# Optimization experiments

Hardware: AMD Instinct MI355X
Metric: run time of the kernel (lower is better)

Reference implementation:

```python
import jax, jax.numpy as jnp
import numpy as np

N = 100000      # nodes
E = 1600000     # edges (avg degree 16)
D_IN = 128
D_OUT = 128


def setup_inputs() -> dict:
    key = jax.random.key(0)
    k_x, k_e, k_w1, k_w2 = jax.random.split(key, 4)
    x = jax.random.normal(k_x, (N, D_IN), dtype=jnp.float32)
    edge_index = jax.random.randint(k_e, (2, E), 0, N, dtype=jnp.int64)
    # xavier_uniform for Linear weights, zero biases (as in reset_parameters)
    lim1 = float(np.sqrt(6.0 / (D_IN + D_OUT)))
    lim2 = float(np.sqrt(6.0 / (D_OUT + D_OUT)))
    W1 = jax.random.uniform(k_w1, (D_IN, D_OUT), jnp.float32, -lim1, lim1)
    b1 = jnp.zeros((D_OUT,), jnp.float32)
    W2 = jax.random.uniform(k_w2, (D_OUT, D_OUT), jnp.float32, -lim2, lim2)
    b2 = jnp.zeros((D_OUT,), jnp.float32)
    eps = jnp.zeros((1,), jnp.float32)  # trainable eps, init 0
    return {"x": x, "edge_index": edge_index, "W1": W1, "b1": b1,
            "W2": W2, "b2": b2, "eps": eps}


def reference(x, edge_index, W1, b1, W2, b2, eps):
    src, dst = edge_index[0], edge_index[1]
    # adj_t.matmul(x): agg[i] = sum_{j in N(i)} x[j]  (gather + scatter-add)
    agg = jax.ops.segment_sum(x[src], dst, num_segments=N)  # [N, D_IN]
    h = (1.0 + eps) * x + agg                                 # eps residual
    h = jax.nn.relu(h @ W1 + b1)                              # Linear + ReLU
    return h @ W2 + b2                                        # Linear
```

## Files before the change

### kernel.cpp

```cpp
#include <hip/hip_runtime.h>

#define DFEAT 128
#define NA 512
#define CELLW 20
#define CAPAB 19
#define MAXBKT 512
#define CAPH 2560
#define OVCAP 32768

typedef __attribute__((ext_vector_type(8))) short short8v;
typedef __attribute__((ext_vector_type(4))) float f32x4;
typedef __attribute__((ext_vector_type(4))) unsigned short ushort4v;

__device__ __forceinline__ unsigned short f2bf(float f) {
    union { float f; unsigned u; } cv; cv.f = f;
    unsigned u = cv.u + 0x7fffu + ((cv.u >> 16) & 1u);
    return (unsigned short)(u >> 16);
}
__device__ __forceinline__ float bf2f(unsigned short h) {
    union { unsigned u; float f; } cv; cv.u = ((unsigned)h) << 16; return cv.f;
}
__device__ __forceinline__ int load_idx(const void* eiv, int is64, size_t i) {
    return is64 ? (int)((const long long*)eiv)[i] : ((const int*)eiv)[i];
}

__global__ __launch_bounds__(256) void prep_kernel(
        const float* __restrict__ W1, const float* __restrict__ W2,
        unsigned short* __restrict__ w1bf, unsigned short* __restrict__ w2bf,
        const float* __restrict__ x, unsigned short* __restrict__ xb, int total4,
        const void* __restrict__ eiv,
        unsigned* __restrict__ gbuf, int* __restrict__ ovcnt,
        int2* __restrict__ ov,
        int E, int N, int nbkt) {
    const int b = blockIdx.x;

    if (b < NA) {
        __shared__ unsigned lcnt[MAXBKT];
        __shared__ unsigned lbuf[MAXBKT * CELLW];

        const int* e32 = (const int*)eiv;
        int orsum = 0;
#pragma unroll
        for (int i = 0; i < 128; ++i) orsum |= e32[2 * i + 1];
        const int is64 = (orsum == 0);

        for (int w = threadIdx.x; w < nbkt; w += 256) lcnt[w] = 0;
        __syncthreads();

        const int chunk = (E + NA - 1) / NA;
        const int e0 = b * chunk;
        const int eEnd = min(e0 + chunk, E);
        for (int e = e0 + threadIdx.x; e < eEnd; e += 256) {
            int src = load_idx(eiv, is64, (size_t)e);
            int dst = load_idx(eiv, is64, (size_t)E + e);
            int bkt = dst >> 8;
            unsigned dl = (unsigned)(dst & 255);
            unsigned pos = atomicAdd(&lcnt[bkt], 1u);
            if (pos < CAPAB)
                lbuf[bkt * CELLW + 1 + pos] = (dl << 17) | (unsigned)src;
            else {
                int o = atomicAdd(ovcnt, 1);
                if (o < OVCAP) ov[o] = make_int2(dst, src);
            }
        }
        __syncthreads();
        for (int w = threadIdx.x; w < nbkt; w += 256)
            lbuf[w * CELLW] = min(lcnt[w], (unsigned)CAPAB);
        __syncthreads();
        const int tot = nbkt * CELLW;
        for (int w = threadIdx.x; w < tot; w += 256) {
            int k = w / CELLW, slot = w - k * CELLW;
            gbuf[((size_t)k * NA + b) * CELLW + slot] = lbuf[w];
        }
    } else if (b < NA + 128) {
        int wb = b - NA;
        const float* W = (wb < 64) ? W1 : W2;
        unsigned short* o = (wb < 64) ? w1bf : w2bf;
        int idx = (wb & 63) * 256 + threadIdx.x;
        int kk = idx >> 7, n = idx & 127;
        o[n * 128 + kk] = f2bf(W[idx]);
    } else {
        int i = (b - NA - 128) * 256 + threadIdx.x;
        if (i < total4) {
            float4 v = *(const float4*)&x[(size_t)i * 4];
            ushort4v o;
            o.x = f2bf(v.x); o.y = f2bf(v.y); o.z = f2bf(v.z); o.w = f2bf(v.w);
            *(ushort4v*)&xb[(size_t)i * 4] = o;
        }
    }
}

__global__ __launch_bounds__(512) void agg_sort_kernel(
        const unsigned short* __restrict__ xb,
        const unsigned* __restrict__ gbuf,
        const int* __restrict__ ovcnt, const int2* __restrict__ ov,
        const float* __restrict__ epsp,
        unsigned short* __restrict__ hb,
        float* __restrict__ hf,
        int N) {
    __shared__ int cnt_s[128];
    __shared__ int scanA[128];
    __shared__ int start_s[129];
    __shared__ int srcS[CAPH];

    const int t = threadIdx.x;
    const int b = blockIdx.x >> 1;
    const int h = blockIdx.x & 1;
    const int node0 = (b << 8) + (h << 7);

    const uint4* cp = (const uint4*)&gbuf[((size_t)b * NA + t) * CELLW];
    uint4 c0 = cp[0], c1 = cp[1], c2 = cp[2], c3 = cp[3], c4 = cp[4];
    unsigned eb[CELLW];
    eb[0]  = c0.x; eb[1]  = c0.y; eb[2]  = c0.z; eb[3]  = c0.w;
    eb[4]  = c1.x; eb[5]  = c1.y; eb[6]  = c1.z; eb[7]  = c1.w;
    eb[8]  = c2.x; eb[9]  = c2.y; eb[10] = c2.z; eb[11] = c2.w;
    eb[12] = c3.x; eb[13] = c3.y; eb[14] = c3.z; eb[15] = c3.w;
    eb[16] = c4.x; eb[17] = c4.y; eb[18] = c4.z; eb[19] = c4.w;
    const int myc = (int)eb[0];

    if (t < 128) cnt_s[t] = 0;
    __syncthreads();
#pragma unroll
    for (int k = 1; k <= CAPAB; ++k)
        if (k <= myc) {
            int dl = (int)(eb[k] >> 17);
            if ((dl >> 7) == h) atomicAdd(&cnt_s[dl & 127], 1);
        }
    __syncthreads();

    if (t < 128) scanA[t] = cnt_s[t];
    __syncthreads();
    for (int off = 1; off < 128; off <<= 1) {
        int v = 0;
        if (t < 128) { v = scanA[t]; if (t >= off) v += scanA[t - off]; }
        __syncthreads();
        if (t < 128) scanA[t] = v;
        __syncthreads();
    }
    if (t < 128) start_s[t + 1] = scanA[t];
    if (t == 0) start_s[0] = 0;
    __syncthreads();
    if (t < 128) cnt_s[t] = start_s[t];
    __syncthreads();

#pragma unroll
    for (int k = 1; k <= CAPAB; ++k)
        if (k <= myc) {
            int dl = (int)(eb[k] >> 17);
            if ((dl >> 7) == h) {
                int pos = atomicAdd(&cnt_s[dl & 127], 1);
                if (pos < CAPH) srcS[pos] = (int)(eb[k] & 0x1FFFFu);
            }
        }
    __syncthreads();

    const int lane = t & 31;
    const int team = t >> 5;
    const int base = t & 32;
    const int c = lane * 4;
    const float epsv = 1.0f + epsp[0];
    const int ovn = min(ovcnt[0], OVCAP);
    const int trips = (ovn + 31) >> 5;

    for (int jj = team; jj < 128; jj += 16) {
        int node = node0 + jj;
        if (node >= N) break;
        int s = start_s[jj];
        int cnt = start_s[jj + 1] - s;

        ushort4v own = *(const ushort4v*)&xb[(size_t)node * DFEAT + c];
        float ax = epsv * bf2f(own.x), ay = epsv * bf2f(own.y);
        float az = epsv * bf2f(own.z), aw = epsv * bf2f(own.w);

        for (int i = 0; i < cnt; i += 16) {
            int rem = cnt - i;
            int sj[16];
#pragma unroll
            for (int q = 0; q < 16; ++q)
                sj[q] = srcS[s + ((i + q < cnt) ? (i + q) : (cnt - 1))];
            ushort4v u[16];
#pragma unroll
            for (int q = 0; q < 16; ++q)
                u[q] = *(const ushort4v*)&xb[(size_t)sj[q] * DFEAT + c];
#pragma unroll
            for (int q = 0; q < 16; ++q) {
                if (rem > q) {
                    ax += bf2f(u[q].x); ay += bf2f(u[q].y);
                    az += bf2f(u[q].z); aw += bf2f(u[q].w);
                }
            }
        }

        for (int tt = 0; tt < trips; ++tt) {
            int j = tt * 32 + lane;
            int2 eo = (j < ovn) ? ov[j] : make_int2(-1, 0);
            unsigned long long bm = __ballot(eo.x == node);
            unsigned m = (unsigned)(bm >> base);
            while (m) {
                int l = __ffs(m) - 1; m &= m - 1;
                int sv = __shfl(eo.y, base + l, 64);
                ushort4v u = *(const ushort4v*)&xb[(size_t)sv * DFEAT + c];
                ax += bf2f(u.x); ay += bf2f(u.y);
                az += bf2f(u.z); aw += bf2f(u.w);
            }
        }

        if (hb) {
            ushort4v hv;
            hv.x = f2bf(ax); hv.y = f2bf(ay); hv.z = f2bf(az); hv.w = f2bf(aw);
            *(ushort4v*)&hb[(size_t)node * DFEAT + c] = hv;
        } else {
            *(float4*)&hf[(size_t)node * DFEAT + c] = make_float4(ax, ay, az, aw);
        }
    }
}

__global__ __launch_bounds__(256) void mlp_mfma_kernel(
        const unsigned short* __restrict__ hb,
        const float* __restrict__ hsrc,
        const unsigned short* __restrict__ w1bf,
        const unsigned short* __restrict__ w2bf,
        const float* __restrict__ b1, const float* __restrict__ b2,
        float* __restrict__ out, int N) {
    __shared__ unsigned short hlds[64 * 136];
    __shared__ unsigned short wlds[128 * 136];

    const int tid  = threadIdx.x;
    const int node0 = blockIdx.x * 64;
    const int lane = tid & 63;
    const int w    = tid >> 6;
    const int l15  = lane & 15;
    const int quad = lane >> 4;

    if (hb) {
        for (int i = tid; i < 64 * 16; i += 256) {
            int m = i >> 4, k0 = (i & 15) * 8;
            int node = node0 + m;
            short8v v = {0, 0, 0, 0, 0, 0, 0, 0};
            if (node < N) v = *(const short8v*)&hb[(size_t)node * DFEAT + k0];
            *(short8v*)&hlds[m * 136 + k0] = v;
        }
    } else {
        for (int i = tid; i < 64 * 32; i += 256) {
            int m = i >> 5, c = (i & 31) * 4;
            int node = node0 + m;
            float4 v = make_float4(0.f, 0.f, 0.f, 0.f);
            if (node < N) v = *(const float4*)&hsrc[(size_t)node * DFEAT + c];
            ushort4v o;
            o.x = f2bf(v.x); o.y = f2bf(v.y); o.z = f2bf(v.z); o.w = f2bf(v.w);
            *(ushort4v*)&hlds[m * 136 + c] = o;
        }
    }
    for (int i = tid; i < 128 * 16; i += 256) {
        int n = i >> 4, k0 = (i & 15) * 8;
        *(short8v*)&wlds[n * 136 + k0] = *(const short8v*)&w1bf[n * 128 + k0];
    }
    __syncthreads();

    const unsigned short* ha = &hlds[(w * 16 + l15) * 136 + quad * 8];

    for (int layer = 0; layer < 2; ++layer) {
        if (layer == 1) {
            __syncthreads();
            for (int i = tid; i < 128 * 16; i += 256) {
                int n = i >> 4, k0 = (i & 15) * 8;
                *(short8v*)&wlds[n * 136 + k0] = *(const short8v*)&w2bf[n * 128 + k0];
            }
            __syncthreads();
        }

        f32x4 acc[8];
#pragma unroll
        for (int nt = 0; nt < 8; ++nt) acc[nt] = (f32x4){0.f, 0.f, 0.f, 0.f};

#pragma unroll
        for (int s = 0; s < 4; ++s) {
            short8v a = *(const short8v*)&ha[s * 32];
#pragma unroll
            for (int nt = 0; nt < 8; ++nt) {
                short8v bf = *(const short8v*)&wlds[(nt * 16 + l15) * 136 + quad * 8 + s * 32];
                acc[nt] = __builtin_amdgcn_mfma_f32_16x16x32_bf16(a, bf, acc[nt], 0, 0, 0);
            }
        }

        const float* bias = layer ? b2 : b1;
        if (layer == 0) {
            __syncthreads();
#pragma unroll
            for (int nt = 0; nt < 8; ++nt) {
                float bv = bias[nt * 16 + l15];
#pragma unroll
                for (int r = 0; r < 4; ++r) {
                    float v = fmaxf(acc[nt][r] + bv, 0.f);
                    hlds[(w * 16 + quad * 4 + r) * 136 + nt * 16 + l15] = f2bf(v);
                }
            }
        } else {
#pragma unroll
            for (int nt = 0; nt < 8; ++nt) {
                float bv = bias[nt * 16 + l15];
#pragma unroll
                for (int r = 0; r < 4; ++r) {
                    int node = node0 + w * 16 + quad * 4 + r;
                    if (node < N)
                        out[(size_t)node * DFEAT + nt * 16 + l15] = acc[nt][r] + bv;
                }
            }
        }
    }
}

__global__ void detect_idx_kernel(const int* __restrict__ ei, int* __restrict__ flag) {
    if (threadIdx.x == 0 && blockIdx.x == 0) {
        int orsum = 0;
#pragma unroll
        for (int i = 0; i < 128; ++i) orsum |= ei[2 * i + 1];
        flag[0] = (orsum == 0) ? 1 : 0;
    }
}

__global__ __launch_bounds__(256) void scatter_kernel(
        const float* __restrict__ x, const void* __restrict__ eiv,
        const int* __restrict__ flag, float* __restrict__ agg, int E) {
    unsigned gid = blockIdx.x * 256u + threadIdx.x;
    unsigned e = gid >> 5;
    if (e >= (unsigned)E) return;
    int c = (gid & 31u) * 4;
    int is64 = flag[0];
    int src = load_idx(eiv, is64, (size_t)e);
    int dst = load_idx(eiv, is64, (size_t)E + e);
    float4 v = *(const float4*)&x[(size_t)src * DFEAT + c];
    float* p = &agg[(size_t)dst * DFEAT + c];
    unsafeAtomicAdd(p + 0, v.x);
    unsafeAtomicAdd(p + 1, v.y);
    unsafeAtomicAdd(p + 2, v.z);
    unsafeAtomicAdd(p + 3, v.w);
}

__global__ __launch_bounds__(256) void mlp_kernel(
        const float* __restrict__ xp,
        const float* __restrict__ W1, const float* __restrict__ b1,
        const float* __restrict__ W2, const float* __restrict__ b2,
        const float* __restrict__ epsp, float* __restrict__ out) {
    __shared__ float hs[32][DFEAT];
    __shared__ float Wc[64][DFEAT];

    const int tid = threadIdx.x;
    const int node0 = blockIdx.x * 32;
    const float epsv = 1.0f + epsp[0];

    for (int i = tid; i < 32 * (DFEAT / 4); i += 256) {
        int n = i >> 5;
        int c = (i & 31) * 4;
        size_t off = (size_t)(node0 + n) * DFEAT + c;
        float4 h = *(const float4*)&out[off];
        float4 xv = *(const float4*)&xp[off];
        h.x += epsv * xv.x; h.y += epsv * xv.y;
        h.z += epsv * xv.z; h.w += epsv * xv.w;
        *(float4*)&hs[n][c] = h;
    }

    const int og = (tid & 31) * 4;
    const int ng = (tid >> 5) * 4;

    for (int layer = 0; layer < 2; ++layer) {
        const float* W = layer ? W2 : W1;
        const float* b = layer ? b2 : b1;

        float acc[4][4];
#pragma unroll
        for (int j = 0; j < 4; ++j) {
            float bj = b[og + j];
#pragma unroll
            for (int i = 0; i < 4; ++i) acc[i][j] = bj;
        }

        for (int chunk = 0; chunk < 2; ++chunk) {
            __syncthreads();
            for (int i = tid; i < 64 * (DFEAT / 4); i += 256) {
                int r = i >> 5;
                int c = (i & 31) * 4;
                *(float4*)&Wc[r][c] =
                    *(const float4*)&W[(size_t)(chunk * 64 + r) * DFEAT + c];
            }
            __syncthreads();
            const int kb = chunk * 64;
            for (int k = 0; k < 64; k += 4) {
                float4 h4[4], w4[4];
#pragma unroll
                for (int i = 0; i < 4; ++i)
                    h4[i] = *(const float4*)&hs[ng + i][kb + k];
#pragma unroll
                for (int j = 0; j < 4; ++j)
                    w4[j] = *(const float4*)&Wc[k + j][og];
#pragma unroll
                for (int i = 0; i < 4; ++i) {
                    acc[i][0] += h4[i].x * w4[0].x + h4[i].y * w4[1].x
                               + h4[i].z * w4[2].x + h4[i].w * w4[3].x;
                    acc[i][1] += h4[i].x * w4[0].y + h4[i].y * w4[1].y
                               + h4[i].z * w4[2].y + h4[i].w * w4[3].y;
                    acc[i][2] += h4[i].x * w4[0].z + h4[i].y * w4[1].z
                               + h4[i].z * w4[2].z + h4[i].w * w4[3].z;
                    acc[i][3] += h4[i].x * w4[0].w + h4[i].y * w4[1].w
                               + h4[i].z * w4[2].w + h4[i].w * w4[3].w;
                }
            }
        }
        __syncthreads();

        if (layer == 0) {
#pragma unroll
            for (int i = 0; i < 4; ++i) {
                float4 r;
                r.x = fmaxf(acc[i][0], 0.0f);
                r.y = fmaxf(acc[i][1], 0.0f);
                r.z = fmaxf(acc[i][2], 0.0f);
                r.w = fmaxf(acc[i][3], 0.0f);
                *(float4*)&hs[ng + i][og] = r;
            }
        } else {
#pragma unroll
            for (int i = 0; i < 4; ++i) {
                float4 r;
                r.x = acc[i][0]; r.y = acc[i][1];
                r.z = acc[i][2]; r.w = acc[i][3];
                *(float4*)&out[(size_t)(node0 + ng + i) * DFEAT + og] = r;
            }
        }
    }
}

extern "C" void kernel_launch(void* const* d_in, const int* in_sizes, int n_in,
                              void* d_out, int out_size, void* d_ws, size_t ws_size,
                              hipStream_t stream) {
    const float* x   = (const float*)d_in[0];
    const void*  ei  = d_in[1];
    const float* W1  = (const float*)d_in[2];
    const float* b1  = (const float*)d_in[3];
    const float* W2  = (const float*)d_in[4];
    const float* b2  = (const float*)d_in[5];
    const float* eps = (const float*)d_in[6];
    float* out = (float*)d_out;

    const int N = in_sizes[0] / DFEAT;
    const int E = in_sizes[1] / 2;
    const int total4 = N * (DFEAT / 4);
    const int nbkt = (N + 255) >> 8;

    char* p = (char*)d_ws;
    unsigned short* w1bf = (unsigned short*)p;  p += 128 * 128 * 2;
    unsigned short* w2bf = (unsigned short*)p;  p += 128 * 128 * 2;
    unsigned short* xb = (unsigned short*)p;    p += (size_t)N * DFEAT * 2;
    int2* ov = (int2*)p;                        p += (size_t)OVCAP * 8;
    int* ovcnt = (int*)p;                       p += 64;
    unsigned* gbuf = (unsigned*)p;              p += (size_t)nbkt * NA * CELLW * 4;
    size_t need_slim = (size_t)(p - (char*)d_ws);
    unsigned short* hb = (unsigned short*)p;    p += (size_t)N * DFEAT * 2;
    size_t need_full = (size_t)(p - (char*)d_ws);

    if (ws_size >= need_slim && nbkt <= MAXBKT) {
        bool full = (ws_size >= need_full);
        int xbBlocks = (total4 + 255) / 256;

        hipMemsetAsync(ovcnt, 0, 64, stream);
        prep_kernel<<<NA + 128 + xbBlocks, 256, 0, stream>>>(
            W1, W2, w1bf, w2bf, x, xb, total4, ei,
            gbuf, ovcnt, ov, E, N, nbkt);
        agg_sort_kernel<<<nbkt * 2, 512, 0, stream>>>(
            xb, gbuf, ovcnt, ov, eps,
            full ? hb : nullptr, out, N);
        mlp_mfma_kernel<<<(N + 63) / 64, 256, 0, stream>>>(
            full ? hb : nullptr, out, w1bf, w2bf, b1, b2, out, N);
        return;
    }

    int* flag3 = (int*)d_ws;
    detect_idx_kernel<<<1, 64, 0, stream>>>((const int*)ei, flag3);
    hipMemsetAsync(d_out, 0, (size_t)out_size * sizeof(float), stream);
    unsigned total = (unsigned)E * 32u;
    scatter_kernel<<<(total + 255u) / 256u, 256, 0, stream>>>(x, ei, flag3, out, E);
    mlp_kernel<<<N / 32, 256, 0, stream>>>(x, W1, b1, W2, b2, eps, out);
}
```

Baseline: 245.7 us.

## Fuse neighbor aggregation and two-layer MLP into one kernel via LDS

The aggregation kernel now writes each 128-node tile's bf16 aggregated features straight into shared memory. The same block then runs both MFMA linear layers on that tile, and the separate MLP kernel is removed. This drops the global round trip of the intermediate h buffer and one kernel launch. The sort scratch arrays are aliased into the weight buffer so shared memory stays bounded. The cost is about 70KB of LDS per block, which may reduce occupancy during the latency-bound gather phase.

```diff
diff --git a/kernel.cpp b/kernel.cpp
--- a/kernel.cpp
+++ b/kernel.cpp
@@ -90,18 +90,21 @@
     }
 }
 
-__global__ __launch_bounds__(512) void agg_sort_kernel(
+__global__ __launch_bounds__(512) void agg_mlp_kernel(
         const unsigned short* __restrict__ xb,
         const unsigned* __restrict__ gbuf,
         const int* __restrict__ ovcnt, const int2* __restrict__ ov,
         const float* __restrict__ epsp,
-        unsigned short* __restrict__ hb,
-        float* __restrict__ hf,
-        int N) {
-    __shared__ int cnt_s[128];
-    __shared__ int scanA[128];
-    __shared__ int start_s[129];
-    __shared__ int srcS[CAPH];
+        const unsigned short* __restrict__ w1bf,
+        const unsigned short* __restrict__ w2bf,
+        const float* __restrict__ b1, const float* __restrict__ b2,
+        float* __restrict__ out, int N) {
+    __shared__ __align__(16) unsigned short hlds[128 * 136];
+    __shared__ __align__(16) unsigned short wbuf[128 * 136];
+    int* cnt_s   = (int*)wbuf;
+    int* scanA   = cnt_s + 128;
+    int* start_s = scanA + 128;
+    int* srcS    = start_s + 132;
 
     const int t = threadIdx.x;
     const int b = blockIdx.x >> 1;
@@ -154,117 +157,85 @@
         }
     __syncthreads();
 
-    const int lane = t & 31;
-    const int team = t >> 5;
-    const int base = t & 32;
-    const int c = lane * 4;
-    const float epsv = 1.0f + epsp[0];
-    const int ovn = min(ovcnt[0], OVCAP);
-    const int trips = (ovn + 31) >> 5;
-
-    for (int jj = team; jj < 128; jj += 16) {
-        int node = node0 + jj;
-        if (node >= N) break;
-        int s = start_s[jj];
-        int cnt = start_s[jj + 1] - s;
-
-        ushort4v own = *(const ushort4v*)&xb[(size_t)node * DFEAT + c];
-        float ax = epsv * bf2f(own.x), ay = epsv * bf2f(own.y);
-        float az = epsv * bf2f(own.z), aw = epsv * bf2f(own.w);
-
-        for (int i = 0; i < cnt; i += 16) {
-            int rem = cnt - i;
-            int sj[16];
-#pragma unroll
-            for (int q = 0; q < 16; ++q)
-                sj[q] = srcS[s + ((i + q < cnt) ? (i + q) : (cnt - 1))];
-            ushort4v u[16];
-#pragma unroll
-            for (int q = 0; q < 16; ++q)
-                u[q] = *(const ushort4v*)&xb[(size_t)sj[q] * DFEAT + c];
-#pragma unroll
-            for (int q = 0; q < 16; ++q) {
-                if (rem > q) {
-                    ax += bf2f(u[q].x); ay += bf2f(u[q].y);
-                    az += bf2f(u[q].z); aw += bf2f(u[q].w);
+    {
+        const int lane = t & 31;
+        const int team = t >> 5;
+        const int base = t & 32;
+        const int c = lane * 4;
+        const float epsv = 1.0f + epsp[0];
+        const int ovn = min(ovcnt[0], OVCAP);
+        const int trips = (ovn + 31) >> 5;
+
+        for (int jj = team; jj < 128; jj += 16) {
+            int node = node0 + jj;
+            if (node >= N) break;
+            int s = start_s[jj];
+            int cnt = start_s[jj + 1] - s;
+
+            ushort4v own = *(const ushort4v*)&xb[(size_t)node * DFEAT + c];
+            float ax = epsv * bf2f(own.x), ay = epsv * bf2f(own.y);
+            float az = epsv * bf2f(own.z), aw = epsv * bf2f(own.w);
+
+            for (int i = 0; i < cnt; i += 16) {
+                int rem = cnt - i;
+                int sj[16];
+#pragma unroll
+                for (int q = 0; q < 16; ++q)
+                    sj[q] = srcS[s + ((i + q < cnt) ? (i + q) : (cnt - 1))];
+                ushort4v u[16];
+#pragma unroll
+                for (int q = 0; q < 16; ++q)
+                    u[q] = *(const ushort4v*)&xb[(size_t)sj[q] * DFEAT + c];
+#pragma unroll
+                for (int q = 0; q < 16; ++q) {
+                    if (rem > q) {
+                        ax += bf2f(u[q].x); ay += bf2f(u[q].y);
+                        az += bf2f(u[q].z); aw += bf2f(u[q].w);
+                    }
                 }
             }
-        }
-
-        for (int tt = 0; tt < trips; ++tt) {
-            int j = tt * 32 + lane;
-            int2 eo = (j < ovn) ? ov[j] : make_int2(-1, 0);
-            unsigned long long bm = __ballot(eo.x == node);
-            unsigned m = (unsigned)(bm >> base);
-            while (m) {
-                int l = __ffs(m) - 1; m &= m - 1;
-                int sv = __shfl(eo.y, base + l, 64);
-                ushort4v u = *(const ushort4v*)&xb[(size_t)sv * DFEAT + c];
-                ax += bf2f(u.x); ay += bf2f(u.y);
-                az += bf2f(u.z); aw += bf2f(u.w);
-            }
-        }
-
-        if (hb) {
+
+            for (int tt = 0; tt < trips; ++tt) {
+                int j = tt * 32 + lane;
+                int2 eo = (j < ovn) ? ov[j] : make_int2(-1, 0);
+                unsigned long long bm = __ballot(eo.x == node);
+                unsigned m = (unsigned)(bm >> base);
+                while (m) {
+                    int l = __ffs(m) - 1; m &= m - 1;
+                    int sv = __shfl(eo.y, base + l, 64);
+                    ushort4v u = *(const ushort4v*)&xb[(size_t)sv * DFEAT + c];
+                    ax += bf2f(u.x); ay += bf2f(u.y);
+                    az += bf2f(u.z); aw += bf2f(u.w);
+                }
+            }
+
             ushort4v hv;
             hv.x = f2bf(ax); hv.y = f2bf(ay); hv.z = f2bf(az); hv.w = f2bf(aw);
-            *(ushort4v*)&hb[(size_t)node * DFEAT + c] = hv;
-        } else {
-            *(float4*)&hf[(size_t)node * DFEAT + c] = make_float4(ax, ay, az, aw);
-        }
-    }
-}
-
-__global__ __launch_bounds__(256) void mlp_mfma_kernel(
-        const unsigned short* __restrict__ hb,
-        const float* __restrict__ hsrc,
-        const unsigned short* __restrict__ w1bf,
-        const unsigned short* __restrict__ w2bf,
-        const float* __restrict__ b1, const float* __restrict__ b2,
-        float* __restrict__ out, int N) {
-    __shared__ unsigned short hlds[64 * 136];
-    __shared__ unsigned short wlds[128 * 136];
-
-    const int tid  = threadIdx.x;
-    const int node0 = blockIdx.x * 64;
-    const int lane = tid & 63;
-    const int w    = tid >> 6;
-    const int l15  = lane & 15;
-    const int quad = lane >> 4;
-
-    if (hb) {
-        for (int i = tid; i < 64 * 16; i += 256) {
-            int m = i >> 4, k0 = (i & 15) * 8;
-            int node = node0 + m;
-            short8v v = {0, 0, 0, 0, 0, 0, 0, 0};
-            if (node < N) v = *(const short8v*)&hb[(size_t)node * DFEAT + k0];
-            *(short8v*)&hlds[m * 136 + k0] = v;
-        }
-    } else {
-        for (int i = tid; i < 64 * 32; i += 256) {
-            int m = i >> 5, c = (i & 31) * 4;
-            int node = node0 + m;
-            float4 v = make_float4(0.f, 0.f, 0.f, 0.f);
-            if (node < N) v = *(const float4*)&hsrc[(size_t)node * DFEAT + c];
-            ushort4v o;
-            o.x = f2bf(v.x); o.y = f2bf(v.y); o.z = f2bf(v.z); o.w = f2bf(v.w);
-            *(ushort4v*)&hlds[m * 136 + c] = o;
-        }
-    }
-    for (int i = tid; i < 128 * 16; i += 256) {
+            *(ushort4v*)&hlds[jj * 136 + c] = hv;
+        }
+    }
+    __syncthreads();
+
+    for (int i = t; i < 128 * 16; i += 512) {
         int n = i >> 4, k0 = (i & 15) * 8;
-        *(short8v*)&wlds[n * 136 + k0] = *(const short8v*)&w1bf[n * 128 + k0];
-    }
-    __syncthreads();
-
-    const unsigned short* ha = &hlds[(w * 16 + l15) * 136 + quad * 8];
+        *(short8v*)&wbuf[n * 136 + k0] = *(const short8v*)&w1bf[n * 128 + k0];
+    }
+    __syncthreads();
+
+    const int lane64 = t & 63;
+    const int ws   = t >> 6;
+    const int tile = ws >> 2;
+    const int w    = ws & 3;
+    const int l15  = lane64 & 15;
+    const int quad = lane64 >> 4;
+    const unsigned short* ha = &hlds[((tile << 6) + w * 16 + l15) * 136 + quad * 8];
 
     for (int layer = 0; layer < 2; ++layer) {
         if (layer == 1) {
             __syncthreads();
-            for (int i = tid; i < 128 * 16; i += 256) {
+            for (int i = t; i < 128 * 16; i += 512) {
                 int n = i >> 4, k0 = (i & 15) * 8;
-                *(short8v*)&wlds[n * 136 + k0] = *(const short8v*)&w2bf[n * 128 + k0];
+                *(short8v*)&wbuf[n * 136 + k0] = *(const short8v*)&w2bf[n * 128 + k0];
             }
             __syncthreads();
         }
@@ -278,7 +249,7 @@
             short8v a = *(const short8v*)&ha[s * 32];
 #pragma unroll
             for (int nt = 0; nt < 8; ++nt) {
-                short8v bf = *(const short8v*)&wlds[(nt * 16 + l15) * 136 + quad * 8 + s * 32];
+                short8v bf = *(const short8v*)&wbuf[(nt * 16 + l15) * 136 + quad * 8 + s * 32];
                 acc[nt] = __builtin_amdgcn_mfma_f32_16x16x32_bf16(a, bf, acc[nt], 0, 0, 0);
             }
         }
@@ -292,7 +263,7 @@
 #pragma unroll
                 for (int r = 0; r < 4; ++r) {
                     float v = fmaxf(acc[nt][r] + bv, 0.f);
-                    hlds[(w * 16 + quad * 4 + r) * 136 + nt * 16 + l15] = f2bf(v);
+                    hlds[((tile << 6) + w * 16 + quad * 4 + r) * 136 + nt * 16 + l15] = f2bf(v);
                 }
             }
         } else {
@@ -301,7 +272,7 @@
                 float bv = bias[nt * 16 + l15];
 #pragma unroll
                 for (int r = 0; r < 4; ++r) {
-                    int node = node0 + w * 16 + quad * 4 + r;
+                    int node = node0 + (tile << 6) + w * 16 + quad * 4 + r;
                     if (node < N)
                         out[(size_t)node * DFEAT + nt * 16 + l15] = acc[nt][r] + bv;
                 }
@@ -454,23 +425,18 @@
     int2* ov = (int2*)p;                        p += (size_t)OVCAP * 8;
     int* ovcnt = (int*)p;                       p += 64;
     unsigned* gbuf = (unsigned*)p;              p += (size_t)nbkt * NA * CELLW * 4;
-    size_t need_slim = (size_t)(p - (char*)d_ws);
-    unsigned short* hb = (unsigned short*)p;    p += (size_t)N * DFEAT * 2;
-    size_t need_full = (size_t)(p - (char*)d_ws);
-
-    if (ws_size >= need_slim && nbkt <= MAXBKT) {
-        bool full = (ws_size >= need_full);
+    size_t need = (size_t)(p - (char*)d_ws);
+
+    if (ws_size >= need && nbkt <= MAXBKT) {
         int xbBlocks = (total4 + 255) / 256;
 
         hipMemsetAsync(ovcnt, 0, 64, stream);
         prep_kernel<<<NA + 128 + xbBlocks, 256, 0, stream>>>(
             W1, W2, w1bf, w2bf, x, xb, total4, ei,
             gbuf, ovcnt, ov, E, N, nbkt);
-        agg_sort_kernel<<<nbkt * 2, 512, 0, stream>>>(
+        agg_mlp_kernel<<<nbkt * 2, 512, 0, stream>>>(
             xb, gbuf, ovcnt, ov, eps,
-            full ? hb : nullptr, out, N);
-        mlp_mfma_kernel<<<(N + 63) / 64, 256, 0, stream>>>(
-            full ? hb : nullptr, out, w1bf, w2bf, b1, b2, out, N);
+            w1bf, w2bf, b1, b2, out, N);
         return;
     }
 
```

Result: faster. 235.7 us (-4.1%).
